# Optimization experiments

Measured on AMD Instinct MI355X. Metric: run time of the kernel, lower is better.

## Reference

```python
import jax, jax.numpy as jnp
import numpy as np

B, S, E, H = 4, 1024, 1024, 16
D = E // H  # head_dim


def setup_inputs() -> dict:
    key = jax.random.key(0)
    ks = jax.random.split(key, 12)
    s = 1.0 / np.sqrt(E)
    return {
        "value": jax.random.normal(ks[0], (B, S, E), jnp.float32),
        "key_in": jax.random.normal(ks[1], (B, S, E), jnp.float32),
        "query": jax.random.normal(ks[2], (B, S, E), jnp.float32),
        "mask": jax.random.randint(ks[3], (B, 1, 1, S), 0, 2, jnp.int32),
        "Wq": jax.random.normal(ks[4], (E, E), jnp.float32) * s,
        "bq": jnp.zeros((E,), jnp.float32),
        "Wk": jax.random.normal(ks[5], (E, E), jnp.float32) * s,
        "bk": jnp.zeros((E,), jnp.float32),
        "Wv": jax.random.normal(ks[6], (E, E), jnp.float32) * s,
        "bv": jnp.zeros((E,), jnp.float32),
        "Wo": jax.random.normal(ks[7], (E, E), jnp.float32) * s,
        "bo": jnp.zeros((E,), jnp.float32),
    }


def reference(value, key_in, query, mask, Wq, bq, Wk, bk, Wv, bv, Wo, bo):
    b = query.shape[0]
    # torch Linear: y = x @ W.T + b
    Q = (query @ Wq.T + bq).reshape(b, query.shape[1], H, D)
    K = (key_in @ Wk.T + bk).reshape(b, key_in.shape[1], H, D)
    V = (value @ Wv.T + bv).reshape(b, value.shape[1], H, D)
    # scores scaled by 1/sqrt(embed_dim) (faithful to source, not head_dim)
    energy = jnp.einsum("bqhd,bkhd->bhqk", Q, K) / jnp.sqrt(jnp.float32(E))
    energy = jnp.where(mask == 0, jnp.float32(-1e20), energy)
    attention = jax.nn.softmax(energy, axis=-1)
    out = jnp.einsum("bhqk,bkhd->bqhd", attention, V).reshape(b, query.shape[1], E)
    return out @ Wo.T + bo
```

## Files before the change

kernel.cpp:

```cpp
#include <hip/hip_runtime.h>


typedef unsigned short u16;
typedef __bf16 bf16x8 __attribute__((ext_vector_type(8)));
typedef __bf16 bf16x2 __attribute__((ext_vector_type(2)));
typedef short s16x4 __attribute__((ext_vector_type(4)));
typedef float f32x4 __attribute__((ext_vector_type(4)));

struct alignas(8) us4_t { u16 x, y, z, w; };

__device__ __forceinline__ u16 f2bf(float x) {
  unsigned int u = __builtin_bit_cast(unsigned int, x);
  unsigned int r = u + 0x7fffu + ((u >> 16) & 1u);
  return (u16)(r >> 16);
}

__device__ __forceinline__ unsigned int pack2bf(float a, float b) {
#if __has_builtin(__builtin_amdgcn_cvt_pk_bf16_f32)
  bf16x2 r = __builtin_amdgcn_cvt_pk_bf16_f32(a, b);
  return __builtin_bit_cast(unsigned int, r);
#else
  return (unsigned int)f2bf(a) | ((unsigned int)f2bf(b) << 16);
#endif
}

__device__ __forceinline__ f32x4 zero4() {
  f32x4 z; z[0] = 0.f; z[1] = 0.f; z[2] = 0.f; z[3] = 0.f; return z;
}

__device__ __forceinline__ void async_copy16(const void* g, void* l) {
  __builtin_amdgcn_global_load_lds(
      (__attribute__((address_space(1))) void*)(uintptr_t)g,
      (__attribute__((address_space(3))) void*)l, 16, 0, 0);
}

__global__ void fused_cast(const float* __restrict__ q, const float* __restrict__ k,
                           const float* __restrict__ v, const float* __restrict__ wq,
                           const float* __restrict__ wk, const float* __restrict__ wv,
                           const float* __restrict__ wo, const int* __restrict__ mask,
                           u16* __restrict__ qo, u16* __restrict__ ko, u16* __restrict__ vo,
                           u16* __restrict__ wqo, u16* __restrict__ wko, u16* __restrict__ wvo,
                           u16* __restrict__ woo, float* __restrict__ biasf) {
  const int blk = blockIdx.x;
  if (blk >= 16384) {
    int i = (blk - 16384) * 256 + threadIdx.x;
    biasf[i] = mask[i] ? 0.f : -1.4427e20f;
    return;
  }
  const float* src; u16* dst; int off;
  if (blk < 4096)       { src = q;  dst = qo;  off = blk; }
  else if (blk < 8192)  { src = k;  dst = ko;  off = blk - 4096; }
  else if (blk < 12288) { src = v;  dst = vo;  off = blk - 8192; }
  else if (blk < 13312) { src = wq; dst = wqo; off = blk - 12288; }
  else if (blk < 14336) { src = wk; dst = wko; off = blk - 13312; }
  else if (blk < 15360) { src = wv; dst = wvo; off = blk - 14336; }
  else                  { src = wo; dst = woo; off = blk - 15360; }
  const size_t i = (size_t)off * 256 + threadIdx.x;
  float4 f = ((const float4*)src)[i];
  unsigned int lo = pack2bf(f.x, f.y), hi = pack2bf(f.z, f.w);
  unsigned long long pk = (unsigned long long)lo | ((unsigned long long)hi << 32);
  ((unsigned long long*)dst)[i] = pk;
}

template <bool OUT_BF16>
__device__ __forceinline__ void gemm_core(const u16* __restrict__ A,
                                          const u16* __restrict__ Bw,
                                          const float* __restrict__ bias,
                                          void* __restrict__ outp, bool trans) {
  __shared__ u16 lA[128 * 64];
  __shared__ u16 lB[64 * 64];
  const int tid = threadIdx.x;
  const int lane = tid & 63, w = tid >> 6;
  const int wm = w >> 1, wn = w & 1;
  const int quad = lane >> 4, l16 = lane & 15;
  const int rg = lane >> 3, cs = lane & 7;
  const int m0 = blockIdx.y * 128, n0 = blockIdx.x * 64;

  f32x4 acc[4][2];
#pragma unroll
  for (int i = 0; i < 4; ++i)
#pragma unroll
    for (int j = 0; j < 2; ++j) acc[i][j] = zero4();

  for (int it = 0; it < 16; ++it) {
    const int k0 = it * 64;
#pragma unroll
    for (int t = 0; t < 4; ++t) {
      const int row = w * 32 + t * 8 + rg;
      const int c = cs ^ (row & 7);
      async_copy16(A + (size_t)(m0 + row) * 1024 + k0 + c * 8, &lA[(w * 32 + t * 8) * 64]);
    }
#pragma unroll
    for (int t = 0; t < 2; ++t) {
      const int row = w * 16 + t * 8 + rg;
      const int c = cs ^ (row & 7);
      async_copy16(Bw + (size_t)(n0 + row) * 1024 + k0 + c * 8, &lB[(w * 16 + t * 8) * 64]);
    }
    __syncthreads();
#pragma unroll
    for (int kk = 0; kk < 2; ++kk) {
      bf16x8 af[4], bfr[2];
#pragma unroll
      for (int i = 0; i < 4; ++i) {
        const int row = wm * 64 + i * 16 + l16;
        af[i] = *(const bf16x8*)&lA[row * 64 + (((kk * 4 + quad) ^ (row & 7)) * 8)];
      }
#pragma unroll
      for (int j = 0; j < 2; ++j) {
        const int row = wn * 32 + j * 16 + l16;
        bfr[j] = *(const bf16x8*)&lB[row * 64 + (((kk * 4 + quad) ^ (row & 7)) * 8)];
      }
#pragma unroll
      for (int i = 0; i < 4; ++i)
#pragma unroll
        for (int j = 0; j < 2; ++j)
          acc[i][j] = __builtin_amdgcn_mfma_f32_16x16x32_bf16(af[i], bfr[j], acc[i][j], 0, 0, 0);
    }
    __syncthreads();
  }

#pragma unroll
  for (int j = 0; j < 2; ++j) {
    const int cg = n0 + wn * 32 + j * 16 + l16;
    const float bj = bias[cg];
#pragma unroll
    for (int i = 0; i < 4; ++i) {
      const f32x4 v = acc[i][j];
      const int r0 = m0 + wm * 64 + i * 16 + quad * 4;
      if (!trans) {
        if (OUT_BF16) {
          u16* o = (u16*)outp;
#pragma unroll
          for (int r = 0; r < 4; ++r) o[(size_t)(r0 + r) * 1024 + cg] = f2bf(v[r] + bj);
        } else {
          float* o = (float*)outp;
#pragma unroll
          for (int r = 0; r < 4; ++r) o[(size_t)(r0 + r) * 1024 + cg] = v[r] + bj;
        }
      } else {
        u16* o = (u16*)outp;
        const int bh = ((r0 >> 10) << 4) + (cg >> 6);
        const int g  = (r0 & 1023) >> 2;
        const int d  = cg & 63;
        union { us4_t s; unsigned int u[2]; } pk;
        pk.u[0] = pack2bf(v[0] + bj, v[1] + bj);
        pk.u[1] = pack2bf(v[2] + bj, v[3] + bj);
        *(us4_t*)&o[(size_t)bh * 65536 + g * 256 + d * 4] = pk.s;
      }
    }
  }
}

__global__ __launch_bounds__(256, 4) void qkv_gemm(
    const u16* __restrict__ Xq, const u16* __restrict__ Xk, const u16* __restrict__ Xv,
    const u16* __restrict__ Wq, const u16* __restrict__ Wk, const u16* __restrict__ Wv,
    const float* __restrict__ bq, const float* __restrict__ bk, const float* __restrict__ bv,
    u16* __restrict__ Qo, u16* __restrict__ Ko, u16* __restrict__ Vto) {
  const int z = blockIdx.z;
  const u16* A = (z == 0) ? Xq : (z == 1) ? Xk : Xv;
  const u16* W = (z == 0) ? Wq : (z == 1) ? Wk : Wv;
  const float* bias = (z == 0) ? bq : (z == 1) ? bk : bv;
  u16* out = (z == 0) ? Qo : (z == 1) ? Ko : Vto;
  gemm_core<true>(A, W, bias, out, z == 2);
}

__global__ __launch_bounds__(256, 4) void out_gemm(
    const u16* __restrict__ A, const u16* __restrict__ W,
    const float* __restrict__ bias, float* __restrict__ out) {
  gemm_core<false>(A, W, bias, out, false);
}

__global__ __launch_bounds__(256, 4) void attn_kernel(
    const u16* __restrict__ Qb, const u16* __restrict__ Kb, const u16* __restrict__ Vtb,
    const float* __restrict__ biasf, u16* __restrict__ Ob) {
  __shared__ u16 lK[128 * 64];
  __shared__ u16 lV[64 * 128];
  u16* lQ = lV;

  const int tid = threadIdx.x;
  const int lane = tid & 63, w = tid >> 6;
  const int quad = lane >> 4, l16 = lane & 15;
  const int rg = lane >> 3, cs = lane & 7;

  const int flat = blockIdx.x;
  const int xcd = flat & 7, r = flat >> 3;
  const int bh = xcd * 8 + (r & 7), qt = r >> 3;
  const int b = bh >> 4;
  const size_t qkBase = (size_t)b * 1048576 + (size_t)(bh & 15) * 64;
  const size_t vBase = (size_t)bh * 65536;
  const float C = 0.0450842200277982f;
  const float* bp = biasf + b * 1024 + quad * 4;

#pragma unroll
  for (int t = 0; t < 2; ++t) {
    const int row = w * 16 + t * 8 + rg;
    const int c = cs ^ (row & 7);
    async_copy16(Qb + qkBase + (size_t)(qt * 64 + row) * 1024 + c * 8,
                 &lQ[(w * 16 + t * 8) * 64]);
  }
  __syncthreads();

  bf16x8 qf[2];
#pragma unroll
  for (int kk = 0; kk < 2; ++kk) {
    const int row = w * 16 + l16;
    qf[kk] = *(const bf16x8*)&lQ[row * 64 + (((kk * 4 + quad) ^ (row & 7)) * 8)];
  }
  __syncthreads();

  float lsum = 0.f;
  f32x4 oacc[4];
#pragma unroll
  for (int dt = 0; dt < 4; ++dt) oacc[dt] = zero4();

  for (int it = 0; it < 8; ++it) {
    const int k0 = it * 128;
#pragma unroll
    for (int t = 0; t < 4; ++t) {
      const int row = w * 32 + t * 8 + rg;
      const int c = cs ^ (row & 7);
      async_copy16(Kb + qkBase + (size_t)(k0 + row) * 1024 + c * 8,
                   &lK[(w * 32 + t * 8) * 64]);
    }
#pragma unroll
    for (int t = 0; t < 4; ++t) {
      const int o16 = (w * 4 + t) * 512 + lane * 8;
      async_copy16(Vtb + vBase + (size_t)it * 8192 + o16, &lV[(w * 4 + t) * 512]);
    }
    __syncthreads();

    f32x4 sacc[8];
#pragma unroll
    for (int n = 0; n < 8; ++n) sacc[n] = zero4();
#pragma unroll
    for (int kk = 0; kk < 2; ++kk) {
#pragma unroll
      for (int n = 0; n < 8; ++n) {
        const int row = n * 16 + l16;
        bf16x8 kf = *(const bf16x8*)&lK[row * 64 + (((kk * 4 + quad) ^ (row & 7)) * 8)];
        sacc[n] = __builtin_amdgcn_mfma_f32_16x16x32_bf16(kf, qf[kk], sacc[n], 0, 0, 0);
      }
    }

    f32x4 sum4 = zero4();
#pragma unroll
    for (int n = 0; n < 8; ++n) {
      const float4 vb = *(const float4*)&bp[k0 + n * 16];
      sacc[n][0] = __builtin_amdgcn_exp2f(fmaf(sacc[n][0], C, vb.x));
      sacc[n][1] = __builtin_amdgcn_exp2f(fmaf(sacc[n][1], C, vb.y));
      sacc[n][2] = __builtin_amdgcn_exp2f(fmaf(sacc[n][2], C, vb.z));
      sacc[n][3] = __builtin_amdgcn_exp2f(fmaf(sacc[n][3], C, vb.w));
      sum4[0] += sacc[n][0]; sum4[1] += sacc[n][1];
      sum4[2] += sacc[n][2]; sum4[3] += sacc[n][3];
    }
    float rs = (sum4[0] + sum4[1]) + (sum4[2] + sum4[3]);
    rs += __shfl_xor(rs, 16);
    rs += __shfl_xor(rs, 32);
    lsum += rs;

    s16x4 pf[8];
#pragma unroll
    for (int n = 0; n < 8; ++n) {
      union { s16x4 v; unsigned int u[2]; } pu;
      pu.u[0] = pack2bf(sacc[n][0], sacc[n][1]);
      pu.u[1] = pack2bf(sacc[n][2], sacc[n][3]);
      pf[n] = pu.v;
    }

#pragma unroll
    for (int dt = 0; dt < 4; ++dt) {
      const int dbase = (dt * 16 + l16) * 4;
#pragma unroll
      for (int ks = 0; ks < 8; ++ks) {
        s16x4 vf = *(const s16x4*)&lV[(ks * 4 + quad) * 256 + dbase];
        oacc[dt] = __builtin_amdgcn_mfma_f32_16x16x16bf16_1k(vf, pf[ks], oacc[dt], 0, 0, 0);
      }
    }
    __syncthreads();
  }

  const float inv = 1.f / lsum;
  const int qg = qt * 64 + w * 16 + l16;
#pragma unroll
  for (int dt = 0; dt < 4; ++dt) {
    union { us4_t s; unsigned int u[2]; } pk;
    pk.u[0] = pack2bf(oacc[dt][0] * inv, oacc[dt][1] * inv);
    pk.u[1] = pack2bf(oacc[dt][2] * inv, oacc[dt][3] * inv);
    *(us4_t*)&Ob[qkBase + (size_t)qg * 1024 + dt * 16 + quad * 4] = pk.s;
  }
}

extern "C" void kernel_launch(void* const* d_in, const int* in_sizes, int n_in,
                              void* d_out, int out_size, void* d_ws, size_t ws_size,
                              hipStream_t stream) {
  const float* value  = (const float*)d_in[0];
  const float* key_in = (const float*)d_in[1];
  const float* query  = (const float*)d_in[2];
  const int*   mask   = (const int*)d_in[3];
  const float* Wq = (const float*)d_in[4];
  const float* bq = (const float*)d_in[5];
  const float* Wk = (const float*)d_in[6];
  const float* bk = (const float*)d_in[7];
  const float* Wv = (const float*)d_in[8];
  const float* bv = (const float*)d_in[9];
  const float* Wo = (const float*)d_in[10];
  const float* bo = (const float*)d_in[11];

  u16* ws = (u16*)d_ws;
  u16* q_bf  = ws;
  u16* k_bf  = ws + 4194304;
  u16* v_bf  = ws + 8388608;
  u16* wq_bf = ws + 12582912;
  u16* wk_bf = ws + 13631488;
  u16* wv_bf = ws + 14680064;
  u16* wo_bf = ws + 15728640;
  u16* Qbuf  = ws + 16777216;
  u16* Kbuf  = ws + 20971520;
  u16* Vtbuf = ws + 25165824;
  u16* attnb = ws + 29360128;
  float* biasf = (float*)d_out;

  fused_cast<<<16400, 256, 0, stream>>>(query, key_in, value, Wq, Wk, Wv, Wo, mask,
                                        q_bf, k_bf, v_bf, wq_bf, wk_bf, wv_bf, wo_bf,
                                        biasf);
  qkv_gemm<<<dim3(16, 32, 3), 256, 0, stream>>>(q_bf, k_bf, v_bf, wq_bf, wk_bf, wv_bf,
                                                bq, bk, bv, Qbuf, Kbuf, Vtbuf);
  attn_kernel<<<dim3(1024), 256, 0, stream>>>(Qbuf, Kbuf, Vtbuf, biasf, attnb);
  out_gemm<<<dim3(16, 32), 256, 0, stream>>>(attnb, wo_bf, bo, (float*)d_out);
}
```

Before: 207.7 us.

## Switch projection GEMMs to 32x32x16 MFMA, larger QKV tiles, XCD-aware block mapping

The projection GEMMs move from 16x16x32 to 32x32x16 bf16 MFMA. The QKV GEMM tile grows from 128x64 to 128x128, so more work is done per shared-memory load. Both GEMMs now use a flat 1D grid with an XCD-aware remapping so neighbouring tiles that share A/B panels land on the same XCD and can reuse its L2. In exchange, the larger accumulators raise register pressure, and launch bounds are lowered to 3 and 2 waves, which cuts occupancy.

Measured after the change: 203.3 us. 2.1% less time.

```diff
diff --git a/kernel.cpp b/kernel.cpp
--- a/kernel.cpp
+++ b/kernel.cpp
@@ -6,6 +6,7 @@
 typedef __bf16 bf16x2 __attribute__((ext_vector_type(2)));
 typedef short s16x4 __attribute__((ext_vector_type(4)));
 typedef float f32x4 __attribute__((ext_vector_type(4)));
+typedef float f32x16 __attribute__((ext_vector_type(16)));
 
 struct alignas(8) us4_t { u16 x, y, z, w; };
 
@@ -62,25 +63,27 @@
   ((unsigned long long*)dst)[i] = pk;
 }
 
-template <bool OUT_BF16>
-__device__ __forceinline__ void gemm_core(const u16* __restrict__ A,
-                                          const u16* __restrict__ Bw,
-                                          const float* __restrict__ bias,
-                                          void* __restrict__ outp, bool trans) {
+template <bool OUT_BF16, int NT>
+__device__ __forceinline__ void gemm_core32(const u16* __restrict__ A,
+                                            const u16* __restrict__ Bw,
+                                            const float* __restrict__ bias,
+                                            void* __restrict__ outp, bool trans,
+                                            int m0, int n0) {
   __shared__ u16 lA[128 * 64];
-  __shared__ u16 lB[64 * 64];
+  __shared__ u16 lB[NT * 64 * 64];
   const int tid = threadIdx.x;
   const int lane = tid & 63, w = tid >> 6;
   const int wm = w >> 1, wn = w & 1;
-  const int quad = lane >> 4, l16 = lane & 15;
+  const int l32 = lane & 31, hi = lane >> 5;
   const int rg = lane >> 3, cs = lane & 7;
-  const int m0 = blockIdx.y * 128, n0 = blockIdx.x * 64;
-
-  f32x4 acc[4][2];
-#pragma unroll
-  for (int i = 0; i < 4; ++i)
-#pragma unroll
-    for (int j = 0; j < 2; ++j) acc[i][j] = zero4();
+
+  f32x16 acc[2][NT];
+#pragma unroll
+  for (int i = 0; i < 2; ++i)
+#pragma unroll
+    for (int j = 0; j < NT; ++j)
+#pragma unroll
+      for (int e = 0; e < 16; ++e) acc[i][j][e] = 0.f;
 
   for (int it = 0; it < 16; ++it) {
     const int k0 = it * 64;
@@ -91,83 +94,96 @@
       async_copy16(A + (size_t)(m0 + row) * 1024 + k0 + c * 8, &lA[(w * 32 + t * 8) * 64]);
     }
 #pragma unroll
-    for (int t = 0; t < 2; ++t) {
-      const int row = w * 16 + t * 8 + rg;
+    for (int t = 0; t < NT * 2; ++t) {
+      const int row = w * (NT * 16) + t * 8 + rg;
       const int c = cs ^ (row & 7);
-      async_copy16(Bw + (size_t)(n0 + row) * 1024 + k0 + c * 8, &lB[(w * 16 + t * 8) * 64]);
+      async_copy16(Bw + (size_t)(n0 + row) * 1024 + k0 + c * 8,
+                   &lB[(w * (NT * 16) + t * 8) * 64]);
     }
     __syncthreads();
 #pragma unroll
-    for (int kk = 0; kk < 2; ++kk) {
-      bf16x8 af[4], bfr[2];
-#pragma unroll
-      for (int i = 0; i < 4; ++i) {
-        const int row = wm * 64 + i * 16 + l16;
-        af[i] = *(const bf16x8*)&lA[row * 64 + (((kk * 4 + quad) ^ (row & 7)) * 8)];
-      }
-#pragma unroll
-      for (int j = 0; j < 2; ++j) {
-        const int row = wn * 32 + j * 16 + l16;
-        bfr[j] = *(const bf16x8*)&lB[row * 64 + (((kk * 4 + quad) ^ (row & 7)) * 8)];
-      }
-#pragma unroll
-      for (int i = 0; i < 4; ++i)
-#pragma unroll
-        for (int j = 0; j < 2; ++j)
-          acc[i][j] = __builtin_amdgcn_mfma_f32_16x16x32_bf16(af[i], bfr[j], acc[i][j], 0, 0, 0);
+    for (int s = 0; s < 4; ++s) {
+      bf16x8 af[2], bfr[NT];
+#pragma unroll
+      for (int i = 0; i < 2; ++i) {
+        const int row = wm * 64 + i * 32 + l32;
+        af[i] = *(const bf16x8*)&lA[row * 64 + (((s * 2 + hi) ^ (row & 7)) * 8)];
+      }
+#pragma unroll
+      for (int j = 0; j < NT; ++j) {
+        const int row = wn * (NT * 32) + j * 32 + l32;
+        bfr[j] = *(const bf16x8*)&lB[row * 64 + (((s * 2 + hi) ^ (row & 7)) * 8)];
+      }
+#pragma unroll
+      for (int i = 0; i < 2; ++i)
+#pragma unroll
+        for (int j = 0; j < NT; ++j)
+          acc[i][j] = __builtin_amdgcn_mfma_f32_32x32x16_bf16(af[i], bfr[j], acc[i][j], 0, 0, 0);
     }
     __syncthreads();
   }
 
 #pragma unroll
-  for (int j = 0; j < 2; ++j) {
-    const int cg = n0 + wn * 32 + j * 16 + l16;
+  for (int j = 0; j < NT; ++j) {
+    const int cg = n0 + wn * (NT * 32) + j * 32 + l32;
     const float bj = bias[cg];
 #pragma unroll
-    for (int i = 0; i < 4; ++i) {
-      const f32x4 v = acc[i][j];
-      const int r0 = m0 + wm * 64 + i * 16 + quad * 4;
-      if (!trans) {
-        if (OUT_BF16) {
+    for (int i = 0; i < 2; ++i) {
+      const int mbase = m0 + wm * 64 + i * 32 + 4 * hi;
+#pragma unroll
+      for (int g = 0; g < 4; ++g) {
+        const int r0 = mbase + 8 * g;
+        if (!trans) {
+          if (OUT_BF16) {
+            u16* o = (u16*)outp;
+#pragma unroll
+            for (int rr = 0; rr < 4; ++rr)
+              o[(size_t)(r0 + rr) * 1024 + cg] = f2bf(acc[i][j][g * 4 + rr] + bj);
+          } else {
+            float* o = (float*)outp;
+#pragma unroll
+            for (int rr = 0; rr < 4; ++rr)
+              o[(size_t)(r0 + rr) * 1024 + cg] = acc[i][j][g * 4 + rr] + bj;
+          }
+        } else {
           u16* o = (u16*)outp;
-#pragma unroll
-          for (int r = 0; r < 4; ++r) o[(size_t)(r0 + r) * 1024 + cg] = f2bf(v[r] + bj);
-        } else {
-          float* o = (float*)outp;
-#pragma unroll
-          for (int r = 0; r < 4; ++r) o[(size_t)(r0 + r) * 1024 + cg] = v[r] + bj;
+          const int bh = ((r0 >> 10) << 4) + (cg >> 6);
+          const int g2 = (r0 & 1023) >> 2;
+          const int d  = cg & 63;
+          union { us4_t s; unsigned int u[2]; } pk;
+          pk.u[0] = pack2bf(acc[i][j][g * 4 + 0] + bj, acc[i][j][g * 4 + 1] + bj);
+          pk.u[1] = pack2bf(acc[i][j][g * 4 + 2] + bj, acc[i][j][g * 4 + 3] + bj);
+          *(us4_t*)&o[(size_t)bh * 65536 + g2 * 256 + d * 4] = pk.s;
         }
-      } else {
-        u16* o = (u16*)outp;
-        const int bh = ((r0 >> 10) << 4) + (cg >> 6);
-        const int g  = (r0 & 1023) >> 2;
-        const int d  = cg & 63;
-        union { us4_t s; unsigned int u[2]; } pk;
-        pk.u[0] = pack2bf(v[0] + bj, v[1] + bj);
-        pk.u[1] = pack2bf(v[2] + bj, v[3] + bj);
-        *(us4_t*)&o[(size_t)bh * 65536 + g * 256 + d * 4] = pk.s;
-      }
-    }
-  }
-}
-
-__global__ __launch_bounds__(256, 4) void qkv_gemm(
+      }
+    }
+  }
+}
+
+__global__ __launch_bounds__(256, 3) void qkv_gemm(
     const u16* __restrict__ Xq, const u16* __restrict__ Xk, const u16* __restrict__ Xv,
     const u16* __restrict__ Wq, const u16* __restrict__ Wk, const u16* __restrict__ Wv,
     const float* __restrict__ bq, const float* __restrict__ bk, const float* __restrict__ bv,
     u16* __restrict__ Qo, u16* __restrict__ Ko, u16* __restrict__ Vto) {
-  const int z = blockIdx.z;
+  const int flat = blockIdx.x;
+  const int xcd = flat & 7, t = flat >> 3;
+  const int n = t & 7, bandl = t >> 3;
+  const int band = xcd * 12 + bandl;
+  const int z = band >> 5, m = band & 31;
   const u16* A = (z == 0) ? Xq : (z == 1) ? Xk : Xv;
   const u16* W = (z == 0) ? Wq : (z == 1) ? Wk : Wv;
   const float* bias = (z == 0) ? bq : (z == 1) ? bk : bv;
   u16* out = (z == 0) ? Qo : (z == 1) ? Ko : Vto;
-  gemm_core<true>(A, W, bias, out, z == 2);
-}
-
-__global__ __launch_bounds__(256, 4) void out_gemm(
+  gemm_core32<true, 2>(A, W, bias, out, z == 2, m * 128, n * 128);
+}
+
+__global__ __launch_bounds__(256, 2) void out_gemm(
     const u16* __restrict__ A, const u16* __restrict__ W,
     const float* __restrict__ bias, float* __restrict__ out) {
-  gemm_core<false>(A, W, bias, out, false);
+  const int flat = blockIdx.x;
+  const int xcd = flat & 7, t = flat >> 3;
+  const int n = t & 15, m = xcd * 4 + (t >> 4);
+  gemm_core32<false, 1>(A, W, bias, out, false, m * 128, n * 64);
 }
 
 __global__ __launch_bounds__(256, 4) void attn_kernel(
@@ -323,8 +339,8 @@
   fused_cast<<<16400, 256, 0, stream>>>(query, key_in, value, Wq, Wk, Wv, Wo, mask,
                                         q_bf, k_bf, v_bf, wq_bf, wk_bf, wv_bf, wo_bf,
                                         biasf);
-  qkv_gemm<<<dim3(16, 32, 3), 256, 0, stream>>>(q_bf, k_bf, v_bf, wq_bf, wk_bf, wv_bf,
-                                                bq, bk, bv, Qbuf, Kbuf, Vtbuf);
+  qkv_gemm<<<dim3(768), 256, 0, stream>>>(q_bf, k_bf, v_bf, wq_bf, wk_bf, wv_bf,
+                                          bq, bk, bv, Qbuf, Kbuf, Vtbuf);
   attn_kernel<<<dim3(1024), 256, 0, stream>>>(Qbuf, Kbuf, Vtbuf, biasf, attnb);
-  out_gemm<<<dim3(16, 32), 256, 0, stream>>>(attnb, wo_bf, bo, (float*)d_out);
-}
+  out_gemm<<<dim3(512), 256, 0, stream>>>(attnb, wo_bf, bo, (float*)d_out);
+}
```
